# Kernel optimization log

Measured on AMD Instinct MI355X. Metric: run time of the kernel, lower is better.

The kernel has to match this reference:

```python
import jax, jax.numpy as jnp
import numpy as np

B, T, D = 2, 2048, 1024   # batch, seq_len, d_model
R, RS = 64, 16            # feature-mixing rank, DPLR sequence-mixing rank

_PARAM_SHAPES = [
    # LowRankFeatureMixing (qk gate path): q, m_gate, k projections (rank-R)
    ("qk_Wq1", (D, R)), ("qk_Wq2", (R, D)), ("qk_Wm1", (D, R)), ("qk_Wm2", (R, D)), ("qk_Wk1", (D, R)), ("qk_Wk2", (R, D)),
    # LowRankFeatureMixing (qk scale path, HyperGLU)
    ("qks_Wq1", (D, R)), ("qks_Wq2", (R, D)), ("qks_Wm1", (D, R)), ("qks_Wm2", (R, D)), ("qks_Wk1", (D, R)), ("qks_Wk2", (R, D)),
    # LowRankFeatureMixing (vo / readout path): v, m_vo projections + static W_O
    ("vo_Wv1", (D, R)), ("vo_Wv2", (R, D)), ("vo_Wm1", (D, R)), ("vo_Wm2", (R, D)), ("vo_Wo", (D, D)),
    # DPLRSequenceMixing 1 (gate): diag + low-rank factors generated from x
    ("sm1_Wd", (D, 1)), ("sm1_Wa", (D, RS)), ("sm1_Wb", (D, RS)),
    # DPLRSequenceMixing 1 (scale, HyperGLU)
    ("sm1s_Wd", (D, 1)), ("sm1s_Wa", (D, RS)), ("sm1s_Wb", (D, RS)),
    # DPLRSequenceMixing 2 (readout)
    ("sm2_Wd", (D, 1)), ("sm2_Wa", (D, RS)), ("sm2_Wb", (D, RS)),
]


def setup_inputs() -> dict:
    key = jax.random.key(0)
    keys = jax.random.split(key, len(_PARAM_SHAPES) + 1)
    inp = {"x": jax.random.normal(keys[0], (B, T, D), dtype=jnp.float32)}
    for k, (name, shape) in zip(keys[1:], _PARAM_SHAPES):
        scale = shape[0] ** -0.5
        inp[name] = jax.random.normal(k, shape, dtype=jnp.float32) * scale
    return inp


def _lowrank(x, Wa, Wb):
    # x: [b,t,d] -> [b,t,d] via rank-R factorization
    return (x @ Wa) @ Wb


def _dplr_mix(x, z, Wd, Wa, Wb):
    """Apply R(x) = diag(d(x)) + A(x) B(x)^T on the kv axis of z [b,tq,tkv]."""
    d = x @ Wd                       # [b,t,1] data-dependent diagonal
    A = x @ Wa                       # [b,t,rs]
    Bm = x @ Wb                      # [b,t,rs]
    zB = jnp.einsum('bij,bjr->bir', z, Bm)          # [b,t,rs]
    return z * jnp.swapaxes(d, 1, 2) + jnp.einsum('bir,bjr->bij', zB, A)


def reference(x, qk_Wq1, qk_Wq2, qk_Wm1, qk_Wm2, qk_Wk1, qk_Wk2,
              qks_Wq1, qks_Wq2, qks_Wm1, qks_Wm2, qks_Wk1, qks_Wk2,
              vo_Wv1, vo_Wv2, vo_Wm1, vo_Wm2, vo_Wo,
              sm1_Wd, sm1_Wa, sm1_Wb, sm1s_Wd, sm1s_Wa, sm1s_Wb,
              sm2_Wd, sm2_Wa, sm2_Wb):
    # Feature mixing (gate, scale, vo paths)
    q  = _lowrank(x, qk_Wq1, qk_Wq2);   mg  = _lowrank(x, qk_Wm1, qk_Wm2);   k  = _lowrank(x, qk_Wk1, qk_Wk2)
    qs = _lowrank(x, qks_Wq1, qks_Wq2); mgs = _lowrank(x, qks_Wm1, qks_Wm2); ks = _lowrank(x, qks_Wk1, qks_Wk2)
    v  = _lowrank(x, vo_Wv1, vo_Wv2);   mvo = _lowrank(x, vo_Wm1, vo_Wm2)

    # QK-like scores, [b,t,t]
    z  = jnp.einsum('bid,bjd->bij', q * mg, k)
    zs = jnp.einsum('bid,bjd->bij', qs * mgs, ks)

    # First DPLR sequence mixing + L2-norm over kv axis (gate branch)
    h_mix = _dplr_mix(x, z, sm1_Wd, sm1_Wa, sm1_Wb)
    h_mix = h_mix / (jnp.linalg.norm(h_mix, axis=-1, keepdims=True) + 1e-8)
    # Scale branch (HyperGLU)
    h_scale = _dplr_mix(x, zs, sm1s_Wd, sm1s_Wa, sm1s_Wb)
    h = jax.nn.softplus(h_scale) * jax.nn.relu(h_mix)

    # Second DPLR mixing -> readout weights, then context + output projection
    readout = _dplr_mix(x, h, sm2_Wd, sm2_Wa, sm2_Wb)      # [b,t,t]
    context = jnp.einsum('bij,bjd->bid', readout, v)        # [b,t,d]
    return (context * mvo) @ vo_Wo.T
```

## Files before the change

### kernel.cpp

```cpp
#include <hip/hip_runtime.h>
#include <math.h>

#define BB 2
#define TT 2048
#define DD 1024
#define RS 16
#define MT (BB*TT)
#define GLD 640
#define KAUG 1056

typedef __attribute__((ext_vector_type(8))) short s16x8;
typedef __attribute__((ext_vector_type(4))) float f32x4;

__device__ __forceinline__ short f2bf(float f) {
    union { float f; unsigned u; } v; v.f = f;
    unsigned r = (v.u + 0x7fffu + ((v.u >> 16) & 1u)) >> 16;
    return (short)r;
}
__device__ __forceinline__ float bf2f(short s) {
    union { unsigned u; float f; } v; v.u = ((unsigned)(unsigned short)s) << 16;
    return v.f;
}

__device__ __forceinline__ void gload16(const void* g, void* l) {
    __builtin_amdgcn_global_load_lds((const __attribute__((address_space(1))) void*)g,
                                     (__attribute__((address_space(3))) void*)l, 16, 0, 0);
}

__device__ __forceinline__ void xcd_swz(int& bx, int& by, int& bz)
{
    const int gx = gridDim.x, gy = gridDim.y;
    const int n = gx * gy * (int)gridDim.z;
    int flat = (bz * gy + by) * gx + bx;
    const int cpx = n >> 3;
    flat = (flat & 7) * cpx + (flat >> 3);
    bx = flat % gx; by = (flat / gx) % gy; bz = flat / (gx * gy);
}

__device__ __forceinline__ void gemm_core128p(const short* __restrict__ A,
                                              const short* __restrict__ Bt,
                                              int K, int lda, int ldb,
                                              int bi, int bj, short* smem,
                                              f32x4 (&acc)[4][4])
{
    const int tid = threadIdx.x;
    const int wv = tid >> 6, lane = tid & 63;
    const int wr = (wv >> 1) * 64, wc = (wv & 1) * 64;

#pragma unroll
    for (int m = 0; m < 4; ++m)
#pragma unroll
        for (int n = 0; n < 4; ++n) acc[m][n] = (f32x4){0.f, 0.f, 0.f, 0.f};

    const int srow = wv * 16 + (lane >> 2);
    const int sg   = ((lane & 3) ^ ((srow >> 1) & 3)) * 8;
    const int frow = lane & 15;
    const int gidx = lane >> 4;
    const int koff = (gidx ^ ((frow >> 1) & 3)) * 8;

    const int nt = K >> 5;
    const long arow = (long)(bi + srow) * lda + sg;
    const long brow = (long)(bj + srow) * ldb + sg;

    auto stage = [&](int t, int q) {
        short* As = smem + q * 8192;
        short* Bs = As + 4096;
        const int k0 = t << 5;
#pragma unroll
        for (int p = 0; p < 2; ++p) {
            gload16(A + arow + (long)p * 64 * lda + k0, As + p*2048 + wv*512);
            gload16(Bt + brow + (long)p * 64 * ldb + k0, Bs + p*2048 + wv*512);
        }
    };

    stage(0, 0);
    if (nt > 1) stage(1, 1);

    for (int t = 0; t < nt; ++t) {
        const int q = t & 1;
        if (t + 1 < nt) asm volatile("s_waitcnt vmcnt(4)" ::: "memory");
        else            asm volatile("s_waitcnt vmcnt(0)" ::: "memory");
        __builtin_amdgcn_s_barrier();

        const short* As = smem + q * 8192;
        const short* Bs = As + 4096;
        s16x8 af[4], bfr[4];
#pragma unroll
        for (int m = 0; m < 4; ++m)
            af[m] = *(const s16x8*)&As[(wr + m*16 + frow) * 32 + koff];
#pragma unroll
        for (int n = 0; n < 4; ++n)
            bfr[n] = *(const s16x8*)&Bs[(wc + n*16 + frow) * 32 + koff];
        asm volatile("s_waitcnt lgkmcnt(0)" ::: "memory");
        __builtin_amdgcn_sched_barrier(0);
        __builtin_amdgcn_s_barrier();

        if (t + 2 < nt) stage(t + 2, q);

#pragma unroll
        for (int m = 0; m < 4; ++m)
#pragma unroll
            for (int n = 0; n < 4; ++n)
                acc[m][n] = __builtin_amdgcn_mfma_f32_16x16x32_bf16(af[m], bfr[n], acc[m][n], 0, 0, 0);
    }
}

template<int STORE>
__global__ __launch_bounds__(256)
void gemm_nt(const short* __restrict__ A, const short* __restrict__ Bt,
             void* __restrict__ Cv, int K, int lda, int ldb, int ldc,
             long sA, long sB, long sC)
{
    int bx = blockIdx.x, by = blockIdx.y, bz = blockIdx.z;
    xcd_swz(bx, by, bz);
    const short* Ab = A  + (long)bz * sA;
    const short* Bb = Bt + (long)bz * sB;
    const int bi = by * 128, bj = bx * 128;
    __shared__ __align__(16) short smem[16384];
    f32x4 acc[4][4];
    gemm_core128p(Ab, Bb, K, lda, ldb, bi, bj, smem, acc);

    const int lane = threadIdx.x & 63, wv = threadIdx.x >> 6;
    const int wr = (wv >> 1) * 64, wc = (wv & 1) * 64;
    const int col0 = lane & 15, row0 = (lane >> 4) * 4;
#pragma unroll
    for (int m = 0; m < 4; ++m)
#pragma unroll
        for (int n = 0; n < 4; ++n)
#pragma unroll
            for (int r = 0; r < 4; ++r) {
                int i = bi + wr + m*16 + row0 + r;
                int j = bj + wc + n*16 + col0;
                if (STORE == 0)
                    ((float*)Cv + (long)bz * sC)[(long)i * ldc + j] = acc[m][n][r];
                else
                    ((short*)Cv + (long)bz * sC)[(long)i * ldc + j] = f2bf(acc[m][n][r]);
            }
}

__global__ __launch_bounds__(256)
void gemm_s1(const short* __restrict__ xb, const short* __restrict__ WcatT,
             short* __restrict__ Gb512,
             float* __restrict__ d1, float* __restrict__ d1s, float* __restrict__ d2,
             float* __restrict__ B1T, float* __restrict__ B1sT, float* __restrict__ A2T,
             short* __restrict__ B2T,
             short* __restrict__ QGaug, short* __restrict__ QSGaug,
             short* __restrict__ KBaug, short* __restrict__ KSBaug)
{
    int bx = blockIdx.x, by = blockIdx.y, bz = blockIdx.z;
    xcd_swz(bx, by, bz);
    const int bi = by * 128, bj = bx * 128;
    __shared__ __align__(16) short smem[16384];
    f32x4 acc[4][4];
    gemm_core128p(xb, WcatT, DD, DD, DD, bi, bj, smem, acc);

    const int lane = threadIdx.x & 63, wv = threadIdx.x >> 6;
    const int wr = (wv >> 1) * 64, wc = (wv & 1) * 64;
    const int col0 = lane & 15, row0 = (lane >> 4) * 4;
#pragma unroll
    for (int m = 0; m < 4; ++m)
#pragma unroll
        for (int n = 0; n < 4; ++n)
#pragma unroll
            for (int r = 0; r < 4; ++r) {
                int i = bi + wr + m*16 + row0 + r;
                int j = bj + wc + n*16 + col0;
                float val = acc[m][n][r];
                if (j < 512) {
                    Gb512[(long)i * 512 + j] = f2bf(val);
                } else if (j == 512) {
                    d1[i] = val;
                    for (int q = 0; q < RS; ++q) {
                        QGaug [(long)i * KAUG + 1040 + q] = 0;
                        QSGaug[(long)i * KAUG + 1040 + q] = 0;
                        KBaug [(long)i * KAUG + 1040 + q] = 0;
                        KSBaug[(long)i * KAUG + 1040 + q] = 0;
                    }
                } else if (j < 529) {
                    KBaug[(long)i * KAUG + 1024 + (j - 513)] = f2bf(val);
                } else if (j < 545) {
                    B1T[(long)(j - 529) * MT + i] = val;
                } else if (j == 545) {
                    d1s[i] = val;
                } else if (j < 562) {
                    KSBaug[(long)i * KAUG + 1024 + (j - 546)] = f2bf(val);
                } else if (j < 578) {
                    B1sT[(long)(j - 562) * MT + i] = val;
                } else if (j == 578) {
                    d2[i] = val;
                } else if (j < 595) {
                    A2T[(long)(j - 579) * MT + i] = val;
                } else if (j < 611) {
                    B2T[(long)(j - 595) * MT + i] = f2bf(val);
                }
            }
}

__global__ __launch_bounds__(256)
void e_kernel(const short* __restrict__ Gb512, const float* __restrict__ BT0,
              float* __restrict__ E)
{
    const int tc = blockIdx.x, b = blockIdx.y, kind = blockIdx.z;
    const int col0 = (kind == 0) ? 128 : (kind == 1) ? 320 : 384;
    const float* BT = BT0 + (size_t)kind * RS * MT;
    const int c = threadIdx.x & 63, rg = threadIdx.x >> 6;
    float acc[4] = {0.f, 0.f, 0.f, 0.f};
    const int t0 = tc * (TT / 16);
#pragma unroll 2
    for (int tt = 0; tt < TT / 16; ++tt) {
        const long gi = (long)b * TT + t0 + tt;
        float g = bf2f(Gb512[gi * 512 + col0 + c]);
#pragma unroll
        for (int q = 0; q < 4; ++q)
            acc[q] = fmaf(g, BT[(long)(rg * 4 + q) * MT + gi], acc[q]);
    }
#pragma unroll
    for (int q = 0; q < 4; ++q)
        atomicAdd(&E[(((long)kind * BB + b) * 64 + c) * RS + rg * 4 + q], acc[q]);
}

__global__ __launch_bounds__(256)
void c1w_kernel(const short* __restrict__ W2, const float* __restrict__ E,
                float* __restrict__ C1, float* __restrict__ A2tV)
{
    const int d0 = blockIdx.x * 64, kind = blockIdx.y, b = blockIdx.z;
    const int s = (kind == 0) ? 2 : (kind == 1) ? 5 : 6;
    __shared__ float El[64][RS];
    {
        const float* Eb = E + ((long)kind * BB + b) * 64 * RS;
        int q = threadIdx.x;
#pragma unroll
        for (int k = 0; k < 4; ++k) ((float*)El)[q + 256 * k] = Eb[q + 256 * k];
    }
    __syncthreads();
    const int dl = threadIdx.x & 63, rg = threadIdx.x >> 6;
    const int d = d0 + dl;
    const short* wrow = W2 + ((long)s * DD + d) * 64;
    float acc[4] = {0.f, 0.f, 0.f, 0.f};
#pragma unroll
    for (int c8 = 0; c8 < 8; ++c8) {
        s16x8 wv = *(const s16x8*)&wrow[c8 * 8];
#pragma unroll
        for (int u = 0; u < 8; ++u) {
            float w = bf2f(wv[u]);
#pragma unroll
            for (int q = 0; q < 4; ++q)
                acc[q] = fmaf(w, El[c8 * 8 + u][rg * 4 + q], acc[q]);
        }
    }
    if (kind < 2) {
        float* dst = C1 + (size_t)kind * BB * DD * RS;
#pragma unroll
        for (int q = 0; q < 4; ++q)
            dst[((long)b * DD + d) * RS + rg * 4 + q] = acc[q];
    } else {
#pragma unroll
        for (int q = 0; q < 4; ++q)
            A2tV[((long)b * RS + rg * 4 + q) * DD + d] = acc[q];
    }
}

__global__ __launch_bounds__(256)
void hmhs_kernel(const short* __restrict__ QGaug, const short* __restrict__ QSGaug,
                 const short* __restrict__ KBaug, const short* __restrict__ KSBaug,
                 short* __restrict__ P, float* __restrict__ rowsum)
{
    int bx = blockIdx.x, by = blockIdx.y, bz = blockIdx.z;
    xcd_swz(bx, by, bz);
    const int b = bz;
    const int bi = by * 128, bj = bx * 128;
    __shared__ __align__(16) short smem[16384];
    f32x4 acc[4][4], acc2[4][4];
    gemm_core128p(QGaug  + (long)b * TT * KAUG, KBaug  + (long)b * TT * KAUG,
                  KAUG, KAUG, KAUG, bi, bj, smem, acc);
    gemm_core128p(QSGaug + (long)b * TT * KAUG, KSBaug + (long)b * TT * KAUG,
                  KAUG, KAUG, KAUG, bi, bj, smem, acc2);

    const int lane = threadIdx.x & 63, wv = threadIdx.x >> 6;
    const int wr = (wv >> 1) * 64, wc = (wv & 1) * 64;
    const int col0 = lane & 15, row0 = (lane >> 4) * 4;
    short* Pb = P + (long)b * TT * TT;

    float ss[4][4];
#pragma unroll
    for (int m = 0; m < 4; ++m)
#pragma unroll
        for (int r = 0; r < 4; ++r) ss[m][r] = 0.f;

#pragma unroll
    for (int m = 0; m < 4; ++m)
#pragma unroll
        for (int n = 0; n < 4; ++n)
#pragma unroll
            for (int r = 0; r < 4; ++r) {
                int i = bi + wr + m*16 + row0 + r;
                int j = bj + wc + n*16 + col0;
                float hmv = acc[m][n][r];
                float sv  = acc2[m][n][r];
                float sp  = fmaxf(sv, 0.f) + __logf(1.f + __expf(-fabsf(sv)));
                Pb[(long)i * TT + j] = f2bf(sp * fmaxf(hmv, 0.f));
                ss[m][r] = fmaf(hmv, hmv, ss[m][r]);
            }

#pragma unroll
    for (int m = 0; m < 4; ++m)
#pragma unroll
        for (int r = 0; r < 4; ++r) {
            float v = ss[m][r];
            v += __shfl_xor(v, 1, 64);
            v += __shfl_xor(v, 2, 64);
            v += __shfl_xor(v, 4, 64);
            v += __shfl_xor(v, 8, 64);
            if (col0 == 0)
                atomicAdd(&rowsum[(long)b * TT + bi + wr + m*16 + row0 + r], v);
        }
}

__global__ __launch_bounds__(256)
void finish_kernel(const short* __restrict__ P, const short* __restrict__ B2T,
                   const float* __restrict__ rowsum, float* __restrict__ hB)
{
    const int i = blockIdx.x, b = blockIdx.y, tid = threadIdx.x;
    const long gi = (long)b * TT + i;
    const float inv = 1.f / (sqrtf(rowsum[gi]) + 1e-8f);
    const short* Pr = P + ((long)b * TT + i) * TT;
    const long tb = (long)b * TT;
    const int j0 = tid * 8;

    float hb[RS];
#pragma unroll
    for (int r = 0; r < RS; ++r) hb[r] = 0.f;

    s16x8 pv = *(const s16x8*)&Pr[j0];
    float pf[8];
#pragma unroll
    for (int q = 0; q < 8; ++q) pf[q] = bf2f(pv[q]);
#pragma unroll
    for (int r = 0; r < RS; ++r) {
        s16x8 bv = *(const s16x8*)&B2T[(long)r * MT + tb + j0];
#pragma unroll
        for (int q = 0; q < 8; ++q) hb[r] = fmaf(pf[q], bf2f(bv[q]), hb[r]);
    }
#pragma unroll
    for (int r = 0; r < RS; ++r)
#pragma unroll
        for (int off = 32; off; off >>= 1) hb[r] += __shfl_down(hb[r], off, 64);
    __shared__ float red[4][RS];
    if ((tid & 63) == 0)
#pragma unroll
        for (int r = 0; r < RS; ++r) red[tid >> 6][r] = hb[r];
    __syncthreads();
    if (tid < RS)
        hB[gi * RS + tid] = (red[0][tid] + red[1][tid] + red[2][tid] + red[3][tid]) * inv;
}

struct S2S { int mode, sa, sb; short* outS; float* outF; const float* rs; };
struct S2A { S2S sl[6]; };

__global__ __launch_bounds__(256)
void stage2_kernel(const short* __restrict__ Gb, const short* __restrict__ W2,
                   S2A args)
{
    int bx = blockIdx.x, by = blockIdx.y, bz = blockIdx.z;
    xcd_swz(bx, by, bz);
    const S2S sl = args.sl[bz];
    const int bi = by * 128, bj = bx * 128;
    __shared__ __align__(16) short smem[16384];
    f32x4 acc[4][4];
    gemm_core128p(Gb + sl.sa * 64, W2 + (long)sl.sa * DD * 64, 64, 512, 64, bi, bj, smem, acc);
    f32x4 acc2[4][4];
    if (sl.mode == 0)
        gemm_core128p(Gb + sl.sb * 64, W2 + (long)sl.sb * DD * 64, 64, 512, 64, bi, bj, smem, acc2);

    const int lane = threadIdx.x & 63, wv = threadIdx.x >> 6;
    const int wr = (wv >> 1) * 64, wc = (wv & 1) * 64;
    const int col0 = lane & 15, row0 = (lane >> 4) * 4;
#pragma unroll
    for (int m = 0; m < 4; ++m)
#pragma unroll
        for (int n = 0; n < 4; ++n)
#pragma unroll
            for (int r = 0; r < 4; ++r) {
                int i = bi + wr + m*16 + row0 + r;
                int j = bj + wc + n*16 + col0;
                float val = acc[m][n][r];
                if (sl.mode == 0) {
                    sl.outS[(long)i * KAUG + j] = f2bf(val * acc2[m][n][r]);
                } else if (sl.mode == 1) {
                    sl.outS[(long)i * KAUG + j] = f2bf(val * sl.rs[i]);
                } else if (sl.mode == 2) {
                    sl.outF[(long)i * DD + j] = val;
                } else {
                    sl.outS[(long)i * DD + j] = f2bf(val);
                }
            }
}

__global__ __launch_bounds__(256)
void ctx_kernel(const short* __restrict__ P, const short* __restrict__ VDT,
                const float* __restrict__ mvo, const float* __restrict__ hB,
                const float* __restrict__ A2tV, const float* __restrict__ rowsum,
                short* __restrict__ cm)
{
    int bx = blockIdx.x, by = blockIdx.y, bz = blockIdx.z;
    xcd_swz(bx, by, bz);
    const int b = bz;
    const int bi = by * 128, bj = bx * 128;
    __shared__ __align__(16) short smem[16384];
    f32x4 acc[4][4];
    gemm_core128p(P + (long)b * TT * TT, VDT + (long)b * DD * TT, TT, TT, TT, bi, bj, smem, acc);

    const int lane = threadIdx.x & 63, wv = threadIdx.x >> 6;
    const int wr = (wv >> 1) * 64, wc = (wv & 1) * 64;
    const int col0 = lane & 15, row0 = (lane >> 4) * 4;
    const float* a2 = A2tV + (long)b * RS * DD;

#pragma unroll
    for (int m = 0; m < 4; ++m)
#pragma unroll
        for (int r = 0; r < 4; ++r) {
            long gi = (long)b * TT + bi + wr + m*16 + row0 + r;
            float iv = 1.f / (sqrtf(rowsum[gi]) + 1e-8f);
#pragma unroll
            for (int n = 0; n < 4; ++n) acc[m][n][r] *= iv;
        }

#pragma unroll
    for (int r16 = 0; r16 < RS; ++r16) {
        float a2v[4];
#pragma unroll
        for (int n = 0; n < 4; ++n)
            a2v[n] = a2[(long)r16 * DD + bj + wc + n*16 + col0];
#pragma unroll
        for (int m = 0; m < 4; ++m)
#pragma unroll
            for (int r = 0; r < 4; ++r) {
                long gi = (long)b * TT + bi + wr + m*16 + row0 + r;
                float hb = hB[gi * RS + r16];
#pragma unroll
                for (int n = 0; n < 4; ++n)
                    acc[m][n][r] = fmaf(hb, a2v[n], acc[m][n][r]);
            }
    }
#pragma unroll
    for (int m = 0; m < 4; ++m)
#pragma unroll
        for (int n = 0; n < 4; ++n)
#pragma unroll
            for (int r = 0; r < 4; ++r) {
                long gi = (long)b * TT + bi + wr + m*16 + row0 + r;
                int j = bj + wc + n*16 + col0;
                cm[gi * DD + j] = f2bf(acc[m][n][r] * mvo[gi * DD + j]);
            }
}

struct ConcatArgs { const float* p[17]; int col0[17]; int wid[17]; };

__global__ __launch_bounds__(256)
void concat_w1_kernel(ConcatArgs a, short* __restrict__ WcatT,
                      float* __restrict__ zp, int zn)
{
    const int q = blockIdx.x * 256 + threadIdx.x;
    if (q < zn) zp[q] = 0.f;
    const int n = blockIdx.x;
    int s = -1, c = 0;
    for (int i = 0; i < 17; ++i)
        if (n >= a.col0[i] && n < a.col0[i] + a.wid[i]) { s = i; c = n - a.col0[i]; }
    for (int k = threadIdx.x; k < DD; k += 256)
        WcatT[(long)n * DD + k] = (s < 0) ? (short)0 : f2bf(a.p[s][(long)k * a.wid[s] + c]);
}

struct Ptrs8 { const float* p[8]; };

__global__ __launch_bounds__(256)
void concat_w2_kernel(Ptrs8 a, short* __restrict__ W2catT)
{
    const int s = blockIdx.y, n0 = blockIdx.x * 64;
    const int tx = threadIdx.x & 63, ty = threadIdx.x >> 6;
    __shared__ float t[64][65];
    const float* W2 = a.p[s];
    for (int kk = ty; kk < 64; kk += 4) t[kk][tx] = W2[(long)kk * DD + n0 + tx];
    __syncthreads();
    for (int n = ty; n < 64; n += 4)
        W2catT[((long)s * DD + n0 + n) * 64 + tx] = f2bf(t[tx][n]);
}

__global__ __launch_bounds__(256)
void f2bf_vec_kernel(const float* __restrict__ in, short* __restrict__ o, long n4)
{
    long i = (long)blockIdx.x * 256 + threadIdx.x;
    if (i < n4) {
        float4 v = ((const float4*)in)[i];
        short4 r; r.x = f2bf(v.x); r.y = f2bf(v.y); r.z = f2bf(v.z); r.w = f2bf(v.w);
        ((short4*)o)[i] = r;
    }
}

__global__ __launch_bounds__(256)
void zb_kernel(short* __restrict__ aug0, const float* __restrict__ C10)
{
    const int gi = blockIdx.x, path = blockIdx.y, b = gi >> 11, tid = threadIdx.x;
    short* aug = aug0 + (size_t)path * MT * KAUG;
    const float* c1 = C10 + (size_t)path * BB * DD * RS + (long)b * DD * RS;
    const short* qrow = aug + (long)gi * KAUG;
    float acc[RS];
#pragma unroll
    for (int r = 0; r < RS; ++r) acc[r] = 0.f;
#pragma unroll
    for (int c = 0; c < 4; ++c) {
        int d = tid + 256 * c;
        float q = bf2f(qrow[d]);
        const float* cr = c1 + (long)d * RS;
#pragma unroll
        for (int r = 0; r < RS; ++r) acc[r] = fmaf(q, cr[r], acc[r]);
    }
#pragma unroll
    for (int r = 0; r < RS; ++r)
#pragma unroll
        for (int off = 32; off; off >>= 1) acc[r] += __shfl_down(acc[r], off, 64);
    __shared__ float red[4][RS];
    if ((tid & 63) == 0)
#pragma unroll
        for (int r = 0; r < RS; ++r) red[tid >> 6][r] = acc[r];
    __syncthreads();
    if (tid < RS)
        aug[(long)gi * KAUG + 1024 + tid] =
            f2bf(red[0][tid] + red[1][tid] + red[2][tid] + red[3][tid]);
}

__global__ __launch_bounds__(256)
void vdt_kernel(const short* __restrict__ v, const float* __restrict__ d2,
                short* __restrict__ o)
{
    const int t0 = blockIdx.x * 32, d0 = blockIdx.y * 32, b = blockIdx.z;
    const int tx = threadIdx.x & 31, ty = threadIdx.x >> 5;
    __shared__ float tile[32][33];
    for (int s = 0; s < 32; s += 8) {
        int t = t0 + ty + s;
        tile[ty + s][tx] = bf2f(v[((long)b * TT + t) * DD + d0 + tx]) * d2[(long)b * TT + t];
    }
    __syncthreads();
    for (int s = 0; s < 32; s += 8) {
        int d = d0 + ty + s;
        o[((long)b * DD + d) * TT + t0 + tx] = f2bf(tile[tx][ty + s]);
    }
}

extern "C" void kernel_launch(void* const* d_in, const int* in_sizes, int n_in,
                              void* d_out, int out_size, void* d_ws, size_t ws_size,
                              hipStream_t stream)
{
    (void)in_sizes; (void)n_in; (void)out_size; (void)ws_size;
    const float* x = (const float*)d_in[0];
    const float* W[27];
    for (int i = 1; i < 27; ++i) W[i] = (const float*)d_in[i];
    float* out = (float*)d_out;

    char* ws = (char*)d_ws;
    size_t off = 0;
    auto alloc = [&](size_t bytes) -> void* {
        void* p = ws + off; off += (bytes + 255) & ~(size_t)255; return p;
    };
    short* xb     = (short*)alloc((size_t)MT * DD * 2);
    short* WcatT  = (short*)alloc((size_t)GLD * DD * 2);
    short* W2catT = (short*)alloc((size_t)8 * DD * 64 * 2);
    short* Gb512  = (short*)alloc((size_t)MT * 512 * 2);
    short* Wob    = (short*)alloc((size_t)DD * DD * 2);
    float* S1     = (float*)alloc((size_t)MT * DD * 4);
    short* VB     = (short*)alloc((size_t)MT * DD * 2);
    short* QGaug  = (short*)alloc((size_t)MT * KAUG * 2);
    short* QSGaug = (short*)alloc((size_t)MT * KAUG * 2);
    short* KBaug  = (short*)alloc((size_t)MT * KAUG * 2);
    short* KSBaug = (short*)alloc((size_t)MT * KAUG * 2);
    short* CM     = (short*)alloc((size_t)MT * DD * 2);
    short* P      = (short*)alloc((size_t)BB * TT * TT * 2);
    float* d1   = (float*)alloc((size_t)MT * 4);
    float* d1s  = (float*)alloc((size_t)MT * 4);
    float* d2   = (float*)alloc((size_t)MT * 4);
    float* B1T  = (float*)alloc((size_t)RS * MT * 4);
    float* B1sT = (float*)alloc((size_t)RS * MT * 4);
    float* A2T  = (float*)alloc((size_t)RS * MT * 4);
    short* B2T  = (short*)alloc((size_t)RS * MT * 2);
    float* C1   = (float*)alloc((size_t)BB * DD * RS * 4);
    float* C1s  = (float*)alloc((size_t)BB * DD * RS * 4);
    float* A2tV = (float*)alloc((size_t)BB * RS * DD * 4);
    float* rowsum = (float*)alloc((size_t)MT * 4);
    float* E    = (float*)alloc((size_t)3 * BB * 64 * RS * 4);
    float* hB   = (float*)alloc((size_t)MT * RS * 4);

    short* VDT = xb;
    short* cm  = CM;

    const long n4 = (long)MT * DD / 4;
    const int ZN = MT + 3 * BB * 64 * RS;

    f2bf_vec_kernel<<<n4 / 256, 256, 0, stream>>>(x, xb, n4);
    ConcatArgs ca;
    {
        const int w1idx[8] = {1, 3, 5, 7, 9, 11, 13, 15};
        for (int s = 0; s < 8; ++s) { ca.p[s] = W[w1idx[s]]; ca.col0[s] = s * 64; ca.wid[s] = 64; }
        const int didx[9] = {18, 19, 20, 21, 22, 23, 24, 25, 26};
        const int dcol[9] = {512, 513, 529, 545, 546, 562, 578, 579, 595};
        const int dwid[9] = {1, 16, 16, 1, 16, 16, 1, 16, 16};
        for (int s = 0; s < 9; ++s) { ca.p[8 + s] = W[didx[s]]; ca.col0[8 + s] = dcol[s]; ca.wid[8 + s] = dwid[s]; }
    }
    concat_w1_kernel<<<GLD, 256, 0, stream>>>(ca, WcatT, rowsum, ZN);
    Ptrs8 p8;
    {
        const int w2idx[8] = {2, 4, 6, 8, 10, 12, 14, 16};
        for (int s = 0; s < 8; ++s) p8.p[s] = W[w2idx[s]];
    }
    concat_w2_kernel<<<dim3(DD / 64, 8), 256, 0, stream>>>(p8, W2catT);
    f2bf_vec_kernel<<<((long)DD * DD / 4) / 256, 256, 0, stream>>>(W[17], Wob, (long)DD * DD / 4);

    gemm_s1<<<dim3(GLD / 128, MT / 128, 1), 256, 0, stream>>>(
        xb, WcatT, Gb512, d1, d1s, d2, B1T, B1sT, A2T, B2T,
        QGaug, QSGaug, KBaug, KSBaug);

    e_kernel<<<dim3(16, BB, 3), 256, 0, stream>>>(Gb512, B1T, E);
    c1w_kernel<<<dim3(DD / 64, 3, BB), 256, 0, stream>>>(W2catT, E, C1, A2tV);

    S2A a;
    a.sl[0] = {0, 0, 1, QGaug,  nullptr, nullptr};
    a.sl[1] = {0, 3, 4, QSGaug, nullptr, nullptr};
    a.sl[2] = {1, 2, 0, KBaug,  nullptr, d1};
    a.sl[3] = {1, 5, 0, KSBaug, nullptr, d1s};
    a.sl[4] = {3, 6, 0, VB,     nullptr, nullptr};
    a.sl[5] = {2, 7, 0, nullptr, S1,     nullptr};
    stage2_kernel<<<dim3(DD / 128, MT / 128, 6), 256, 0, stream>>>(Gb512, W2catT, a);

    vdt_kernel<<<dim3(TT / 32, DD / 32, BB), 256, 0, stream>>>(VB, d2, VDT);

    zb_kernel<<<dim3(MT, 2), 256, 0, stream>>>(QGaug, C1);

    hmhs_kernel<<<dim3(TT / 128, TT / 128, BB), 256, 0, stream>>>(
        QGaug, QSGaug, KBaug, KSBaug, P, rowsum);

    finish_kernel<<<dim3(TT, BB), 256, 0, stream>>>(P, B2T, rowsum, hB);

    ctx_kernel<<<dim3(DD / 128, TT / 128, BB), 256, 0, stream>>>(
        P, VDT, S1, hB, A2tV, rowsum, cm);

    gemm_nt<0><<<dim3(DD / 128, MT / 128, 1), 256, 0, stream>>>(
        cm, Wob, out, DD, DD, DD, DD, 0, 0, 0);
}
```

Before: 289.4 us.

## Deepen GEMM LDS pipeline to triple buffering and fuse dual hmhs GEMM loops

Changes the shared GEMM mainloop from double to triple buffering in LDS, prefetching three k-tiles ahead with adjusted vmcnt waits, and grows every kernel's shared buffer to 48KB. Adds a dedicated hmhs_core that runs the two back-to-back augmented GEMMs as one continuous pipelined loop. The prefetch no longer drains and restarts between the two products. The aim is to hide more global-load latency. The larger LDS footprint may lower occupancy, and stage2's very short K=64 loops gain little.

Measured after the change: 369.4 us. 1.28x slower.

```diff
diff --git a/kernel.cpp b/kernel.cpp
--- a/kernel.cpp
+++ b/kernel.cpp
@@ -75,11 +75,14 @@
 
     stage(0, 0);
     if (nt > 1) stage(1, 1);
-
+    if (nt > 2) stage(2, 2);
+
+    int q = 0;
     for (int t = 0; t < nt; ++t) {
-        const int q = t & 1;
-        if (t + 1 < nt) asm volatile("s_waitcnt vmcnt(4)" ::: "memory");
-        else            asm volatile("s_waitcnt vmcnt(0)" ::: "memory");
+        const int rem = nt - 1 - t;
+        if (rem >= 2)      asm volatile("s_waitcnt vmcnt(8)" ::: "memory");
+        else if (rem == 1) asm volatile("s_waitcnt vmcnt(4)" ::: "memory");
+        else               asm volatile("s_waitcnt vmcnt(0)" ::: "memory");
         __builtin_amdgcn_s_barrier();
 
         const short* As = smem + q * 8192;
@@ -95,13 +98,100 @@
         __builtin_amdgcn_sched_barrier(0);
         __builtin_amdgcn_s_barrier();
 
-        if (t + 2 < nt) stage(t + 2, q);
+        if (t + 3 < nt) stage(t + 3, q);
 
 #pragma unroll
         for (int m = 0; m < 4; ++m)
 #pragma unroll
             for (int n = 0; n < 4; ++n)
                 acc[m][n] = __builtin_amdgcn_mfma_f32_16x16x32_bf16(af[m], bfr[n], acc[m][n], 0, 0, 0);
+        q = (q == 2) ? 0 : q + 1;
+    }
+}
+
+#define NTAUG (KAUG >> 5)
+__device__ __forceinline__ void hmhs_core(const short* __restrict__ A1,
+                                          const short* __restrict__ B1,
+                                          const short* __restrict__ A2,
+                                          const short* __restrict__ B2,
+                                          int bi, int bj, short* smem,
+                                          f32x4 (&acc)[4][4], f32x4 (&acc2)[4][4])
+{
+    const int tid = threadIdx.x;
+    const int wv = tid >> 6, lane = tid & 63;
+    const int wr = (wv >> 1) * 64, wc = (wv & 1) * 64;
+
+#pragma unroll
+    for (int m = 0; m < 4; ++m)
+#pragma unroll
+        for (int n = 0; n < 4; ++n) {
+            acc[m][n]  = (f32x4){0.f, 0.f, 0.f, 0.f};
+            acc2[m][n] = (f32x4){0.f, 0.f, 0.f, 0.f};
+        }
+
+    const int srow = wv * 16 + (lane >> 2);
+    const int sg   = ((lane & 3) ^ ((srow >> 1) & 3)) * 8;
+    const int frow = lane & 15;
+    const int gidx = lane >> 4;
+    const int koff = (gidx ^ ((frow >> 1) & 3)) * 8;
+
+    const long arow = (long)(bi + srow) * KAUG + sg;
+    const long brow = (long)(bj + srow) * KAUG + sg;
+    const int NG = 2 * NTAUG;
+
+    auto stage = [&](int g, int q) {
+        const short* Ap = (g < NTAUG) ? A1 : A2;
+        const short* Bp = (g < NTAUG) ? B1 : B2;
+        const int t = (g < NTAUG) ? g : g - NTAUG;
+        short* As = smem + q * 8192;
+        short* Bs = As + 4096;
+        const int k0 = t << 5;
+#pragma unroll
+        for (int p = 0; p < 2; ++p) {
+            gload16(Ap + arow + (long)p * 64 * KAUG + k0, As + p*2048 + wv*512);
+            gload16(Bp + brow + (long)p * 64 * KAUG + k0, Bs + p*2048 + wv*512);
+        }
+    };
+
+    stage(0, 0); stage(1, 1); stage(2, 2);
+
+    int q = 0;
+    for (int g = 0; g < NG; ++g) {
+        const int rem = NG - 1 - g;
+        if (rem >= 2)      asm volatile("s_waitcnt vmcnt(8)" ::: "memory");
+        else if (rem == 1) asm volatile("s_waitcnt vmcnt(4)" ::: "memory");
+        else               asm volatile("s_waitcnt vmcnt(0)" ::: "memory");
+        __builtin_amdgcn_s_barrier();
+
+        const short* As = smem + q * 8192;
+        const short* Bs = As + 4096;
+        s16x8 af[4], bfr[4];
+#pragma unroll
+        for (int m = 0; m < 4; ++m)
+            af[m] = *(const s16x8*)&As[(wr + m*16 + frow) * 32 + koff];
+#pragma unroll
+        for (int n = 0; n < 4; ++n)
+            bfr[n] = *(const s16x8*)&Bs[(wc + n*16 + frow) * 32 + koff];
+        asm volatile("s_waitcnt lgkmcnt(0)" ::: "memory");
+        __builtin_amdgcn_sched_barrier(0);
+        __builtin_amdgcn_s_barrier();
+
+        if (g + 3 < NG) stage(g + 3, q);
+
+        if (g < NTAUG) {
+#pragma unroll
+            for (int m = 0; m < 4; ++m)
+#pragma unroll
+                for (int n = 0; n < 4; ++n)
+                    acc[m][n] = __builtin_amdgcn_mfma_f32_16x16x32_bf16(af[m], bfr[n], acc[m][n], 0, 0, 0);
+        } else {
+#pragma unroll
+            for (int m = 0; m < 4; ++m)
+#pragma unroll
+                for (int n = 0; n < 4; ++n)
+                    acc2[m][n] = __builtin_amdgcn_mfma_f32_16x16x32_bf16(af[m], bfr[n], acc2[m][n], 0, 0, 0);
+        }
+        q = (q == 2) ? 0 : q + 1;
     }
 }
 
@@ -116,7 +206,7 @@
     const short* Ab = A  + (long)bz * sA;
     const short* Bb = Bt + (long)bz * sB;
     const int bi = by * 128, bj = bx * 128;
-    __shared__ __align__(16) short smem[16384];
+    __shared__ __align__(16) short smem[24576];
     f32x4 acc[4][4];
     gemm_core128p(Ab, Bb, K, lda, ldb, bi, bj, smem, acc);
 
@@ -150,7 +240,7 @@
     int bx = blockIdx.x, by = blockIdx.y, bz = blockIdx.z;
     xcd_swz(bx, by, bz);
     const int bi = by * 128, bj = bx * 128;
-    __shared__ __align__(16) short smem[16384];
+    __shared__ __align__(16) short smem[24576];
     f32x4 acc[4][4];
     gemm_core128p(xb, WcatT, DD, DD, DD, bi, bj, smem, acc);
 
@@ -269,12 +359,11 @@
     xcd_swz(bx, by, bz);
     const int b = bz;
     const int bi = by * 128, bj = bx * 128;
-    __shared__ __align__(16) short smem[16384];
+    __shared__ __align__(16) short smem[24576];
     f32x4 acc[4][4], acc2[4][4];
-    gemm_core128p(QGaug  + (long)b * TT * KAUG, KBaug  + (long)b * TT * KAUG,
-                  KAUG, KAUG, KAUG, bi, bj, smem, acc);
-    gemm_core128p(QSGaug + (long)b * TT * KAUG, KSBaug + (long)b * TT * KAUG,
-                  KAUG, KAUG, KAUG, bi, bj, smem, acc2);
+    hmhs_core(QGaug  + (long)b * TT * KAUG, KBaug  + (long)b * TT * KAUG,
+              QSGaug + (long)b * TT * KAUG, KSBaug + (long)b * TT * KAUG,
+              bi, bj, smem, acc, acc2);
 
     const int lane = threadIdx.x & 63, wv = threadIdx.x >> 6;
     const int wr = (wv >> 1) * 64, wc = (wv & 1) * 64;
@@ -365,7 +454,7 @@
     xcd_swz(bx, by, bz);
     const S2S sl = args.sl[bz];
     const int bi = by * 128, bj = bx * 128;
-    __shared__ __align__(16) short smem[16384];
+    __shared__ __align__(16) short smem[24576];
     f32x4 acc[4][4];
     gemm_core128p(Gb + sl.sa * 64, W2 + (long)sl.sa * DD * 64, 64, 512, 64, bi, bj, smem, acc);
     f32x4 acc2[4][4];
@@ -406,7 +495,7 @@
     xcd_swz(bx, by, bz);
     const int b = bz;
     const int bi = by * 128, bj = bx * 128;
-    __shared__ __align__(16) short smem[16384];
+    __shared__ __align__(16) short smem[24576];
     f32x4 acc[4][4];
     gemm_core128p(P + (long)b * TT * TT, VDT + (long)b * DD * TT, TT, TT, TT, bi, bj, smem, acc);
 
```
